# Optimization experiments

Measured on AMD Instinct MI355X. Metric: run time of the kernel, lower is better.

The kernel has to match this reference:

```python
import jax, jax.numpy as jnp
import numpy as np

N, G, E, H, M = 200000, 16, 400000, 400000, 800000
DN, DG, DE, DH, DM = 128, 32, 128, 64, 64
K_EDGE, K_HYP, AK = 32, 3, 8  # fixed incident edges per node, nodes per hyperedge, attention key size / heads
LN_EPS = 1e-3  # keras LayerNormalization default epsilon


def setup_inputs() -> dict:
    key = jax.random.key(0)
    ks = jax.random.split(key, 20)
    p = lambda k, shp: (0.02 * jax.random.normal(k, shp, dtype=jnp.float32))
    return {
        "nodes": jax.random.normal(ks[0], (N, DN), dtype=jnp.float32),
        "globals_": jax.random.normal(ks[1], (G, DG), dtype=jnp.float32),
        "n_node": jnp.full((G,), N // G, dtype=jnp.int32),
        "edges": jax.random.normal(ks[2], (E, DE), dtype=jnp.float32),
        "edge_ind": jax.random.randint(ks[3], (N, K_EDGE), 0, E, dtype=jnp.int32),
        "hfeat": jax.random.normal(ks[4], (H, DH), dtype=jnp.float32),
        "hind": jax.random.randint(ks[5], (H, K_HYP), 0, N, dtype=jnp.int32),
        "mfeat": jax.random.normal(ks[6], (M, DM), dtype=jnp.float32),
        "mind": jax.random.randint(ks[7], (M,), 0, N, dtype=jnp.int32),
        "Wq": p(ks[8], (DN, AK)), "bq": jnp.zeros((AK,), jnp.float32),
        "Wk": p(ks[9], (DE, AK)), "bk": jnp.zeros((AK,), jnp.float32),
        "Wc": p(ks[10], (4, AK, AK)), "bc": jnp.zeros((AK,), jnp.float32),
        "W1": p(ks[11], (DN + DG + AK + DH + DM, 256)), "b1": jnp.zeros((256,), jnp.float32),
        "W2": p(ks[12], (256, 128)), "b2": jnp.zeros((128,), jnp.float32),
        "ln_g": jnp.ones((128,), jnp.float32), "ln_b": jnp.zeros((128,), jnp.float32),
    }


def reference(nodes, globals_, n_node, edges, edge_ind, hfeat, hind, mfeat, mind,
              Wq, bq, Wk, bk, Wc, bc, W1, b1, W2, b2, ln_g, ln_b):
    n = nodes.shape[0]
    # _one_to_segments: repeat globals per node (graph id from n_node offsets)
    gid = jnp.searchsorted(jnp.cumsum(n_node), jnp.arange(n), side="right")
    g_per_node = globals_[gid]  # [N, DG]

    # EDGES branch: fixed-number multi-head attention over incident edges
    q = nodes @ Wq + bq   # [N, AK]
    k = edges @ Wk + bk   # [E, AK]
    # Conv1D(kernel=4, 'same') on a length-1 sequence: only kernel tap 1 touches data
    q_mh = q @ Wc[1] + bc  # [N, heads]
    k_mh = k @ Wc[1] + bc  # [E, heads]
    ek = k_mh[edge_ind]                         # [N, K, heads] gathered keys (= values)
    attn = jax.nn.softmax(q_mh[:, None, :] * ek, axis=1)
    edge_agg = jnp.sum(attn * ek, axis=1)       # [N, heads] (flatten of [N,1,heads])

    # _one_to_fixed_number: scatter hyperedge features to their K_HYP member nodes
    hh, kk, dh = hfeat.shape[0], hind.shape[1], hfeat.shape[1]
    h_agg = jax.ops.segment_sum(
        jnp.broadcast_to(hfeat[:, None, :], (hh, kk, dh)).reshape(hh * kk, dh),
        hind.reshape(-1), num_segments=n)       # [N, DH]

    # _one_to_unsorted_segments
    m_agg = jax.ops.segment_sum(mfeat, mind, num_segments=n)  # [N, DM]

    x = jnp.concatenate([nodes, g_per_node, edge_agg, h_agg, m_agg], axis=1)
    h1 = jax.nn.relu(x @ W1 + b1)
    h2 = jax.nn.relu(h1 @ W2 + b2)
    mu = jnp.mean(h2, axis=-1, keepdims=True)
    var = jnp.var(h2, axis=-1, keepdims=True)
    out = (h2 - mu) * jax.lax.rsqrt(var + LN_EPS) * ln_g + ln_b
    return out
```

## Files before the change

### kernel.cpp

```cpp
#include <hip/hip_runtime.h>
#include <hip/hip_bf16.h>
#include <math.h>

#define N_NODES 200000
#define N_E     400000
#define N_H     400000
#define N_M     800000
#define HK3     1200000
#define DIM_N   128
#define K_EDGE  32
#define D1      296
#define KX      320
#define LN_EPS  1e-3f
#define TILE    32
#define CHUNK   1024
#define NCH     196

typedef __attribute__((ext_vector_type(8))) short bf16x8;
typedef __attribute__((ext_vector_type(4))) float f32x4;
typedef unsigned short ushort_t;

#define SWZ(rr) (((rr) & 7) << 4)

__device__ __forceinline__ short f2bf(float f) {
    unsigned u = __float_as_uint(f);
    unsigned r = (u + 0x7fffu + ((u >> 16) & 1u)) >> 16;
    return (short)r;
}
__device__ __forceinline__ float bf2f(ushort_t u) {
    return __uint_as_float(((unsigned)u) << 16);
}
__device__ __forceinline__ void split2(float v, short& hi, short& lo) {
    hi = f2bf(v);
    float r = v - __uint_as_float(((unsigned)(ushort_t)hi) << 16);
    lo = f2bf(r);
}

__global__ void prep_weights(const float* __restrict__ Wq, const float* __restrict__ bq,
                             const float* __restrict__ Wk, const float* __restrict__ bk,
                             const float* __restrict__ Wc, const float* __restrict__ bc,
                             float* Wqc, float* bqc, float* Wkc, float* bkc) {
    int t = blockIdx.x * 256 + threadIdx.x;
    const float* Wc1 = Wc + 64;
    if (t < 128 * 8) {
        int i = t >> 3, o = t & 7;
        float s = 0.f, s2 = 0.f;
        for (int a = 0; a < 8; ++a) {
            float w = Wc1[a * 8 + o];
            s  += Wq[i * 8 + a] * w;
            s2 += Wk[i * 8 + a] * w;
        }
        Wqc[t] = s;
        Wkc[t] = s2;
    } else if (t < 128 * 8 + 8) {
        int o = t - 1024;
        float s = 0.f, s2 = 0.f;
        for (int a = 0; a < 8; ++a) {
            float w = Wc1[a * 8 + o];
            s  += bq[a] * w;
            s2 += bk[a] * w;
        }
        bqc[o] = s + bc[o];
        bkc[o] = s2 + bc[o];
    }
}

__global__ void prep_wF(const float* __restrict__ W1, const float* __restrict__ W2,
                        short* __restrict__ W1Fh, short* __restrict__ W1Fl,
                        short* __restrict__ W2Fh, short* __restrict__ W2Fl) {
    int g = blockIdx.x * 256 + threadIdx.x;
    if (g < 10240) {
        int l = g & 63, f = g >> 6;
        int s = f % 10, nt = (f / 10) & 3, wid = f / 40;
        int col = wid * 64 + nt * 16 + (l & 15);
        int k0 = s * 32 + (l >> 4) * 8;
        #pragma unroll
        for (int j = 0; j < 8; ++j) {
            int k = k0 + j;
            float w = (k < D1) ? W1[k * 256 + col] : 0.f;
            short hi, lo; split2(w, hi, lo);
            W1Fh[g * 8 + j] = hi; W1Fl[g * 8 + j] = lo;
        }
    } else if (g < 14336) {
        int u = g - 10240;
        int l = u & 63, f = u >> 6;
        int s = f & 7, nt = (f >> 3) & 1, wid = f >> 4;
        int col = wid * 32 + nt * 16 + (l & 15);
        int k0 = s * 32 + (l >> 4) * 8;
        #pragma unroll
        for (int j = 0; j < 8; ++j) {
            float w = W2[(k0 + j) * 128 + col];
            short hi, lo; split2(w, hi, lo);
            W2Fh[u * 8 + j] = hi; W2Fl[u * 8 + j] = lo;
        }
    }
}

__global__ __launch_bounds__(256) void mh_kernel(const float* __restrict__ feat,
                                                 const float* __restrict__ Wf,
                                                 const float* __restrict__ bf_,
                                                 ushort_t* __restrict__ out8) {
    __shared__ __align__(16) float el[32 * 132];
    __shared__ __align__(16) float wlT[8 * 132];
    __shared__ float bl[8];
    int tid = threadIdx.x;
    for (int i = tid; i < 1024; i += 256) {
        int h = i >> 7, k = i & 127;
        wlT[h * 132 + k] = Wf[k * 8 + h];
    }
    if (tid < 8) bl[tid] = bf_[tid];
    long e0 = (long)blockIdx.x * 32;
    const float4* ep = (const float4*)feat + e0 * 32;
    for (int it = 0; it < 4; ++it) {
        int idx = it * 256 + tid;
        int e = idx >> 5, f = idx & 31;
        float4 v = ep[e * 32 + f];
        float* d = &el[e * 132 + f * 4];
        d[0] = v.x; d[1] = v.y; d[2] = v.z; d[3] = v.w;
    }
    __syncthreads();
    int e = tid >> 3, h = tid & 7;
    float acc = bl[h];
    const float* er = &el[e * 132];
    const float* wr = &wlT[h * 132];
    #pragma unroll 8
    for (int i = 0; i < 128; i += 4) {
        float4 ev = *(const float4*)&er[i];
        float4 wv = *(const float4*)&wr[i];
        acc += ev.x * wv.x + ev.y * wv.y + ev.z * wv.z + ev.w * wv.w;
    }
    out8[(e0 + e) * 8 + h] = (ushort_t)f2bf(acc);
}

__global__ void zero_ints(int* __restrict__ p, int n) {
    int stride = gridDim.x * blockDim.x;
    for (int i = blockIdx.x * blockDim.x + threadIdx.x; i < n; i += stride) p[i] = 0;
}

__global__ void count_kernel(const int* __restrict__ hind, const int* __restrict__ mind,
                             int* __restrict__ cnth, int* __restrict__ cntm) {
    int t = blockIdx.x * 256 + threadIdx.x;
    if (t < HK3)              atomicAdd(&cnth[hind[t]], 1);
    else if (t < HK3 + N_M)   atomicAdd(&cntm[mind[t - HK3]], 1);
}

__global__ __launch_bounds__(256) void sum_chunks(const int* __restrict__ cnth,
                                                  const int* __restrict__ cntm,
                                                  int* __restrict__ bsum) {
    int b = blockIdx.x;
    const int* cnt = (b < NCH) ? cnth : cntm;
    int base = ((b < NCH) ? b : b - NCH) * CHUNK;
    int tid = threadIdx.x;
    int s = 0;
    #pragma unroll
    for (int i = 0; i < 4; ++i) {
        int idx = base + i * 256 + tid;
        if (idx < N_NODES) s += cnt[idx];
    }
    __shared__ int sb[4];
    for (int d = 1; d < 64; d <<= 1) s += __shfl_xor(s, d);
    if ((tid & 63) == 0) sb[tid >> 6] = s;
    __syncthreads();
    if (tid == 0) bsum[b] = sb[0] + sb[1] + sb[2] + sb[3];
}

__global__ __launch_bounds__(256) void scan_sums(int* __restrict__ bsum) {
    __shared__ int sh[2][256];
    int tid = threadIdx.x;
    sh[0][tid] = (tid < NCH) ? bsum[tid] : 0;
    sh[1][tid] = (tid < NCH) ? bsum[NCH + tid] : 0;
    __syncthreads();
    for (int d = 1; d < 256; d <<= 1) {
        int v0 = (tid >= d) ? sh[0][tid - d] : 0;
        int v1 = (tid >= d) ? sh[1][tid - d] : 0;
        __syncthreads();
        sh[0][tid] += v0; sh[1][tid] += v1;
        __syncthreads();
    }
    if (tid < NCH) {
        bsum[tid]       = tid ? sh[0][tid - 1] : 0;
        bsum[NCH + tid] = tid ? sh[1][tid - 1] : 0;
    }
}

__global__ __launch_bounds__(256) void scan_chunks(const int* __restrict__ cnth,
                                                   const int* __restrict__ cntm,
                                                   const int* __restrict__ bsum,
                                                   int* __restrict__ offh, int* __restrict__ woffh,
                                                   int* __restrict__ offm, int* __restrict__ woffm) {
    int b = blockIdx.x;
    bool ish = (b < NCH);
    const int* cnt = ish ? cnth : cntm;
    int c = ish ? b : b - NCH;
    int* off  = ish ? offh  : offm;
    int* woff = ish ? woffh : woffm;
    int base = c * CHUNK;
    int tid = threadIdx.x;
    __shared__ int lds[CHUNK];
    __shared__ int tsum[256];
    #pragma unroll
    for (int i = 0; i < 4; ++i) {
        int idx = base + i * 256 + tid;
        lds[i * 256 + tid] = (idx < N_NODES) ? cnt[idx] : 0;
    }
    __syncthreads();
    int v0 = lds[tid * 4], v1 = lds[tid * 4 + 1], v2 = lds[tid * 4 + 2], v3 = lds[tid * 4 + 3];
    int tot = v0 + v1 + v2 + v3;
    tsum[tid] = tot;
    __syncthreads();
    for (int d = 1; d < 256; d <<= 1) {
        int v = (tid >= d) ? tsum[tid - d] : 0;
        __syncthreads();
        tsum[tid] += v;
        __syncthreads();
    }
    int pre = tsum[tid] - tot + bsum[b];
    int4 o;
    o.x = pre; o.y = pre + v0; o.z = pre + v0 + v1; o.w = pre + v0 + v1 + v2;
    int idx = base + tid * 4;
    if (idx + 3 < N_NODES) {
        *(int4*)(off + idx)  = o;
        *(int4*)(woff + idx) = o;
    } else {
        if (idx     < N_NODES) { off[idx]     = o.x; woff[idx]     = o.x; }
        if (idx + 1 < N_NODES) { off[idx + 1] = o.y; woff[idx + 1] = o.y; }
        if (idx + 2 < N_NODES) { off[idx + 2] = o.z; woff[idx + 2] = o.z; }
        if (idx + 3 < N_NODES) { off[idx + 3] = o.w; woff[idx + 3] = o.w; }
    }
}

__global__ void fill_kernel(const int* __restrict__ hind, const int* __restrict__ mind,
                            int* __restrict__ woffh, int* __restrict__ woffm,
                            int* __restrict__ listh, int* __restrict__ listm) {
    int t = blockIdx.x * 256 + threadIdx.x;
    if (t < HK3) {
        int node = hind[t];
        int pos = atomicAdd(&woffh[node], 1);
        listh[pos] = t / 3;
    } else if (t < HK3 + N_M) {
        int m = t - HK3;
        int node = mind[m];
        int pos = atomicAdd(&woffm[node], 1);
        listm[pos] = m;
    }
}

__global__ __launch_bounds__(256) void main_kernel(
    const float* __restrict__ nodes, const float* __restrict__ globals_,
    const int* __restrict__ n_node, const int* __restrict__ edge_ind,
    const ushort_t* __restrict__ kmh, const ushort_t* __restrict__ qmh,
    const float* __restrict__ hfeat, const int* __restrict__ offh,
    const int* __restrict__ woffh, const int* __restrict__ listh,
    const float* __restrict__ mfeat, const int* __restrict__ offm,
    const int* __restrict__ woffm, const int* __restrict__ listm,
    const short* __restrict__ W1Fh, const short* __restrict__ W1Fl, const float* __restrict__ b1,
    const short* __restrict__ W2Fh, const short* __restrict__ W2Fl, const float* __restrict__ b2,
    const float* __restrict__ ln_g, const float* __restrict__ ln_b,
    float* __restrict__ out)
{
    __shared__ __align__(16) char buf[32768];
    __shared__ int eind[32 * 33];
    __shared__ float mrs[64];

    int tid = threadIdx.x;
    int n0 = blockIdx.x * TILE;
    char* xhi = buf;

    const float4* np4 = (const float4*)nodes;
    #pragma unroll
    for (int it = 0; it < 4; ++it) {
        int idx = it * 256 + tid;
        int r = idx >> 5, c4 = idx & 31;
        float4 v = np4[(size_t)(n0 + r) * 32 + c4];
        short4 hi;
        hi.x = f2bf(v.x); hi.y = f2bf(v.y); hi.z = f2bf(v.z); hi.w = f2bf(v.w);
        *(short4*)(xhi + r * 640 + ((c4 * 8) ^ SWZ(r))) = hi;
    }
    {
        int nn0 = n_node[0];
        int r = tid >> 3, c4 = tid & 7;
        int gid = (n0 + r) / nn0;
        float4 v = ((const float4*)globals_)[gid * 8 + c4];
        short4 hi;
        hi.x = f2bf(v.x); hi.y = f2bf(v.y); hi.z = f2bf(v.z); hi.w = f2bf(v.w);
        *(short4*)(xhi + r * 640 + ((256 + c4 * 8) ^ SWZ(r))) = hi;
    }
    {
        int r = tid >> 3, q = tid & 7;
        int n = n0 + r;
        float a[8];
        #pragma unroll
        for (int i = 0; i < 8; ++i) a[i] = 0.f;
        int e0 = offh[n], e1 = woffh[n];
        int e = e0;
        #define ACC8(U, V) do { \
            a[0] += (U).x; a[1] += (U).y; a[2] += (U).z; a[3] += (U).w; \
            a[4] += (V).x; a[5] += (V).y; a[6] += (V).z; a[7] += (V).w; } while (0)
        for (; e + 4 <= e1; e += 4) {
            int i0 = listh[e], i1 = listh[e + 1], i2 = listh[e + 2], i3 = listh[e + 3];
            const float4* p0 = (const float4*)(hfeat + (size_t)i0 * 64 + q * 8);
            const float4* p1 = (const float4*)(hfeat + (size_t)i1 * 64 + q * 8);
            const float4* p2 = (const float4*)(hfeat + (size_t)i2 * 64 + q * 8);
            const float4* p3 = (const float4*)(hfeat + (size_t)i3 * 64 + q * 8);
            float4 u0 = p0[0], v0 = p0[1];
            float4 u1 = p1[0], v1 = p1[1];
            float4 u2 = p2[0], v2 = p2[1];
            float4 u3 = p3[0], v3 = p3[1];
            ACC8(u0, v0); ACC8(u1, v1); ACC8(u2, v2); ACC8(u3, v3);
        }
        for (; e < e1; ++e) {
            const float4* p = (const float4*)(hfeat + (size_t)listh[e] * 64 + q * 8);
            float4 u = p[0], v = p[1];
            ACC8(u, v);
        }
        {
            bf16x8 hi;
            #pragma unroll
            for (int i = 0; i < 8; ++i) hi[i] = f2bf(a[i]);
            *(bf16x8*)(xhi + r * 640 + ((336 + q * 16) ^ SWZ(r))) = hi;
        }
        #pragma unroll
        for (int i = 0; i < 8; ++i) a[i] = 0.f;
        e0 = offm[n]; e1 = woffm[n];
        e = e0;
        for (; e + 4 <= e1; e += 4) {
            int i0 = listm[e], i1 = listm[e + 1], i2 = listm[e + 2], i3 = listm[e + 3];
            const float4* p0 = (const float4*)(mfeat + (size_t)i0 * 64 + q * 8);
            const float4* p1 = (const float4*)(mfeat + (size_t)i1 * 64 + q * 8);
            const float4* p2 = (const float4*)(mfeat + (size_t)i2 * 64 + q * 8);
            const float4* p3 = (const float4*)(mfeat + (size_t)i3 * 64 + q * 8);
            float4 u0 = p0[0], v0 = p0[1];
            float4 u1 = p1[0], v1 = p1[1];
            float4 u2 = p2[0], v2 = p2[1];
            float4 u3 = p3[0], v3 = p3[1];
            ACC8(u0, v0); ACC8(u1, v1); ACC8(u2, v2); ACC8(u3, v3);
        }
        for (; e < e1; ++e) {
            const float4* p = (const float4*)(mfeat + (size_t)listm[e] * 64 + q * 8);
            float4 u = p[0], v = p[1];
            ACC8(u, v);
        }
        #undef ACC8
        {
            bf16x8 hi;
            #pragma unroll
            for (int i = 0; i < 8; ++i) hi[i] = f2bf(a[i]);
            *(bf16x8*)(xhi + r * 640 + ((464 + q * 16) ^ SWZ(r))) = hi;
        }
    }
    if (tid < 192) {
        short4 z = { 0, 0, 0, 0 };
        int r = tid / 6, j = tid % 6;
        *(short4*)(xhi + r * 640 + ((592 + j * 8) ^ SWZ(r))) = z;
    }
    #pragma unroll
    for (int it = 0; it < 4; ++it) {
        int idx = it * 256 + tid;
        int r = idx >> 5, j = idx & 31;
        eind[r * 33 + j] = edge_ind[(size_t)(n0 + r) * 32 + j];
    }
    __syncthreads();

    {
        int r = tid & 31, h = tid >> 5;
        float qv = bf2f(qmh[(size_t)(n0 + r) * 8 + h]);
        float m = -INFINITY, s = 0.f, wv = 0.f;
        for (int j = 0; j < K_EDGE; ++j) {
            int e = eind[r * 33 + j];
            float v = bf2f(kmh[(size_t)e * 8 + h]);
            float l = qv * v;
            float mn = fmaxf(m, l);
            float fac = __expf(m - mn);
            float p = __expf(l - mn);
            s = s * fac + p;
            wv = wv * fac + p * v;
            m = mn;
        }
        *(short*)(xhi + r * 640 + ((320 + h * 2) ^ SWZ(r))) = f2bf(wv / s);
    }
    __syncthreads();

    int wid = tid >> 6, lane = tid & 63;
    int arow = lane & 15, kgrp = lane >> 4;
    f32x4 c1[2][4];
    #pragma unroll
    for (int mt = 0; mt < 2; ++mt)
        #pragma unroll
        for (int nt = 0; nt < 4; ++nt)
            c1[mt][nt] = (f32x4){0.f, 0.f, 0.f, 0.f};
    const bf16x8* w1h = (const bf16x8*)W1Fh;
    const bf16x8* w1l = (const bf16x8*)W1Fl;
    for (int s = 0; s < 10; ++s) {
        int kb = (s * 32 + kgrp * 8) * 2;
        bf16x8 ahv[2], bh[4], bl[4];
        #pragma unroll
        for (int mt = 0; mt < 2; ++mt) {
            int rr = mt * 16 + arow;
            ahv[mt] = *(const bf16x8*)(xhi + rr * 640 + (kb ^ SWZ(rr)));
        }
        #pragma unroll
        for (int nt = 0; nt < 4; ++nt) {
            size_t fi = ((size_t)(wid * 4 + nt) * 10 + s) * 64 + lane;
            bh[nt] = w1h[fi];
            bl[nt] = w1l[fi];
        }
        #pragma unroll
        for (int mt = 0; mt < 2; ++mt)
            #pragma unroll
            for (int nt = 0; nt < 4; ++nt) {
                c1[mt][nt] = __builtin_amdgcn_mfma_f32_16x16x32_bf16(ahv[mt], bh[nt], c1[mt][nt], 0, 0, 0);
                c1[mt][nt] = __builtin_amdgcn_mfma_f32_16x16x32_bf16(ahv[mt], bl[nt], c1[mt][nt], 0, 0, 0);
            }
    }
    __syncthreads();
    char* h1hi = buf;
    char* h1lo = buf + 16384;
    #pragma unroll
    for (int nt = 0; nt < 4; ++nt) {
        int col = wid * 64 + nt * 16 + arow;
        float bb = b1[col];
        #pragma unroll
        for (int mt = 0; mt < 2; ++mt)
            #pragma unroll
            for (int i = 0; i < 4; ++i) {
                int rr = mt * 16 + kgrp * 4 + i;
                float v = fmaxf(c1[mt][nt][i] + bb, 0.f);
                short hi, lo; split2(v, hi, lo);
                int off = rr * 512 + ((col * 2) ^ SWZ(rr));
                *(short*)(h1hi + off) = hi;
                *(short*)(h1lo + off) = lo;
            }
    }
    __syncthreads();

    f32x4 c2[2][2];
    #pragma unroll
    for (int mt = 0; mt < 2; ++mt)
        #pragma unroll
        for (int nt = 0; nt < 2; ++nt)
            c2[mt][nt] = (f32x4){0.f, 0.f, 0.f, 0.f};
    const bf16x8* w2h = (const bf16x8*)W2Fh;
    const bf16x8* w2l = (const bf16x8*)W2Fl;
    for (int s = 0; s < 8; ++s) {
        int kb = (s * 32 + kgrp * 8) * 2;
        bf16x8 ahv[2], alv[2], bh[2], bl[2];
        #pragma unroll
        for (int mt = 0; mt < 2; ++mt) {
            int rr = mt * 16 + arow;
            int off = rr * 512 + (kb ^ SWZ(rr));
            ahv[mt] = *(const bf16x8*)(h1hi + off);
            alv[mt] = *(const bf16x8*)(h1lo + off);
        }
        #pragma unroll
        for (int nt = 0; nt < 2; ++nt) {
            size_t fi = ((size_t)(wid * 2 + nt) * 8 + s) * 64 + lane;
            bh[nt] = w2h[fi];
            bl[nt] = w2l[fi];
        }
        #pragma unroll
        for (int mt = 0; mt < 2; ++mt)
            #pragma unroll
            for (int nt = 0; nt < 2; ++nt) {
                c2[mt][nt] = __builtin_amdgcn_mfma_f32_16x16x32_bf16(ahv[mt], bh[nt], c2[mt][nt], 0, 0, 0);
                c2[mt][nt] = __builtin_amdgcn_mfma_f32_16x16x32_bf16(ahv[mt], bl[nt], c2[mt][nt], 0, 0, 0);
                c2[mt][nt] = __builtin_amdgcn_mfma_f32_16x16x32_bf16(alv[mt], bh[nt], c2[mt][nt], 0, 0, 0);
            }
    }
    __syncthreads();
    #pragma unroll
    for (int nt = 0; nt < 2; ++nt) {
        int col = wid * 32 + nt * 16 + arow;
        float bb = b2[col];
        #pragma unroll
        for (int mt = 0; mt < 2; ++mt)
            #pragma unroll
            for (int i = 0; i < 4; ++i) {
                int rr = mt * 16 + kgrp * 4 + i;
                *(float*)(buf + rr * 528 + col * 4) = fmaxf(c2[mt][nt][i] + bb, 0.f);
            }
    }
    __syncthreads();

    {
        int r = tid >> 3, q = tid & 7;
        const float* row = (const float*)(buf + r * 528) + q * 16;
        float s = 0.f, sq = 0.f;
        #pragma unroll
        for (int j = 0; j < 4; ++j) {
            float4 v = *(const float4*)(row + j * 4);
            s  += v.x + v.y + v.z + v.w;
            sq += v.x * v.x + v.y * v.y + v.z * v.z + v.w * v.w;
        }
        s  += __shfl_xor(s, 1);  sq += __shfl_xor(sq, 1);
        s  += __shfl_xor(s, 2);  sq += __shfl_xor(sq, 2);
        s  += __shfl_xor(s, 4);  sq += __shfl_xor(sq, 4);
        if (q == 0) {
            float mean = s * (1.f / 128.f);
            float var = sq * (1.f / 128.f) - mean * mean;
            mrs[r] = mean;
            mrs[32 + r] = rsqrtf(var + LN_EPS);
        }
    }
    __syncthreads();
    #pragma unroll
    for (int it = 0; it < 4; ++it) {
        int idx = it * 256 + tid;
        int r = idx >> 5, c4 = idx & 31;
        float4 v = *(const float4*)(buf + r * 528 + c4 * 16);
        float mu = mrs[r], rs = mrs[32 + r];
        float4 g = ((const float4*)ln_g)[c4];
        float4 bb = ((const float4*)ln_b)[c4];
        float4 o;
        o.x = (v.x - mu) * rs * g.x + bb.x;
        o.y = (v.y - mu) * rs * g.y + bb.y;
        o.z = (v.z - mu) * rs * g.z + bb.z;
        o.w = (v.w - mu) * rs * g.w + bb.w;
        ((float4*)out)[(size_t)(n0 + r) * 32 + c4] = o;
    }
}

extern "C" void kernel_launch(void* const* d_in, const int* in_sizes, int n_in,
                              void* d_out, int out_size, void* d_ws, size_t ws_size,
                              hipStream_t stream) {
    const float* nodes    = (const float*)d_in[0];
    const float* globals_ = (const float*)d_in[1];
    const int*   n_node   = (const int*)  d_in[2];
    const float* edges    = (const float*)d_in[3];
    const int*   edge_ind = (const int*)  d_in[4];
    const float* hfeat    = (const float*)d_in[5];
    const int*   hind     = (const int*)  d_in[6];
    const float* mfeat    = (const float*)d_in[7];
    const int*   mind     = (const int*)  d_in[8];
    const float* Wq       = (const float*)d_in[9];
    const float* bq       = (const float*)d_in[10];
    const float* Wk       = (const float*)d_in[11];
    const float* bk       = (const float*)d_in[12];
    const float* Wc       = (const float*)d_in[13];
    const float* bc       = (const float*)d_in[14];
    const float* W1       = (const float*)d_in[15];
    const float* b1       = (const float*)d_in[16];
    const float* W2       = (const float*)d_in[17];
    const float* b2       = (const float*)d_in[18];
    const float* ln_g     = (const float*)d_in[19];
    const float* ln_b     = (const float*)d_in[20];
    float* out = (float*)d_out;

    char* w = (char*)d_ws;
    size_t off = 0;
    auto take = [&](size_t bytes) -> char* {
        char* p = w + off;
        off = (off + bytes + 255) & ~(size_t)255;
        return p;
    };
    float*    Wqc  = (float*)take(1024 * 4);
    float*    bqc  = (float*)take(8 * 4);
    float*    Wkc  = (float*)take(1024 * 4);
    float*    bkc  = (float*)take(8 * 4);
    short*    W1Fh = (short*)take(256 * KX * 2);
    short*    W1Fl = (short*)take(256 * KX * 2);
    short*    W2Fh = (short*)take(128 * 256 * 2);
    short*    W2Fl = (short*)take(128 * 256 * 2);
    ushort_t* kmh  = (ushort_t*)take((size_t)N_E * 8 * 2);
    ushort_t* qmh  = (ushort_t*)take((size_t)N_NODES * 8 * 2);
    int*      cnth = (int*)take((size_t)N_NODES * 4);
    int*      cntm = (int*)take((size_t)N_NODES * 4);
    int*      offh = (int*)take((size_t)N_NODES * 4);
    int*      woffh= (int*)take((size_t)N_NODES * 4);
    int*      offm = (int*)take((size_t)N_NODES * 4);
    int*      woffm= (int*)take((size_t)N_NODES * 4);
    int*      listh= (int*)take((size_t)HK3 * 4);
    int*      listm= (int*)take((size_t)N_M * 4);
    int*      bsum = (int*)take(2 * NCH * 4);
    (void)ws_size;

    prep_weights<<<5, 256, 0, stream>>>(Wq, bq, Wk, bk, Wc, bc, Wqc, bqc, Wkc, bkc);
    prep_wF<<<56, 256, 0, stream>>>(W1, W2, W1Fh, W1Fl, W2Fh, W2Fl);
    mh_kernel<<<N_E / 32, 256, 0, stream>>>(edges, Wkc, bkc, kmh);
    mh_kernel<<<N_NODES / 32, 256, 0, stream>>>(nodes, Wqc, bqc, qmh);
    zero_ints<<<512, 256, 0, stream>>>(cnth, 2 * N_NODES);
    count_kernel<<<(HK3 + N_M + 255) / 256, 256, 0, stream>>>(hind, mind, cnth, cntm);
    sum_chunks<<<2 * NCH, 256, 0, stream>>>(cnth, cntm, bsum);
    scan_sums<<<1, 256, 0, stream>>>(bsum);
    scan_chunks<<<2 * NCH, 256, 0, stream>>>(cnth, cntm, bsum, offh, woffh, offm, woffm);
    fill_kernel<<<(HK3 + N_M + 255) / 256, 256, 0, stream>>>(hind, mind, woffh, woffm, listh, listm);
    main_kernel<<<N_NODES / TILE, 256, 0, stream>>>(
        nodes, globals_, n_node, edge_ind, kmh, qmh,
        hfeat, offh, woffh, listh, mfeat, offm, woffm, listm,
        W1Fh, W1Fl, b1, W2Fh, W2Fl, b2, ln_g, ln_b, out);
}
```

Baseline: 713.4 us.

## Fuse projection and count kernels into one launch; drop h1 low-part split

The two per-row head-projection launches and the atomic count launch are merged into one kernel whose blocks are partitioned by index range, so independent work can overlap and launch gaps disappear. Separately, the second MLP layer no longer splits h1 into hi/lo bf16 parts: h1 is stored once as bf16, and one of the three MFMA passes is removed, along with 12KB of shared memory. This cuts LDS traffic, MFMA count and LDS footprint, which may raise occupancy, at the cost of lower precision in the h1 activations.

```diff
diff --git a/kernel.cpp b/kernel.cpp
--- a/kernel.cpp
+++ b/kernel.cpp
@@ -15,6 +15,9 @@
 #define TILE    32
 #define CHUNK   1024
 #define NCH     196
+#define NB_E    12500
+#define NB_N    6250
+#define NB_C    7813
 
 typedef __attribute__((ext_vector_type(8))) short bf16x8;
 typedef __attribute__((ext_vector_type(4))) float f32x4;
@@ -96,20 +99,18 @@
     }
 }
 
-__global__ __launch_bounds__(256) void mh_kernel(const float* __restrict__ feat,
-                                                 const float* __restrict__ Wf,
-                                                 const float* __restrict__ bf_,
-                                                 ushort_t* __restrict__ out8) {
-    __shared__ __align__(16) float el[32 * 132];
-    __shared__ __align__(16) float wlT[8 * 132];
-    __shared__ float bl[8];
-    int tid = threadIdx.x;
+__device__ __forceinline__ void mh_body(const float* __restrict__ feat,
+                                        const float* __restrict__ Wf,
+                                        const float* __restrict__ bf_,
+                                        ushort_t* __restrict__ out8,
+                                        int blk, int tid,
+                                        float* el, float* wlT, float* bl) {
     for (int i = tid; i < 1024; i += 256) {
         int h = i >> 7, k = i & 127;
         wlT[h * 132 + k] = Wf[k * 8 + h];
     }
     if (tid < 8) bl[tid] = bf_[tid];
-    long e0 = (long)blockIdx.x * 32;
+    long e0 = (long)blk * 32;
     const float4* ep = (const float4*)feat + e0 * 32;
     for (int it = 0; it < 4; ++it) {
         int idx = it * 256 + tid;
@@ -132,16 +133,32 @@
     out8[(e0 + e) * 8 + h] = (ushort_t)f2bf(acc);
 }
 
+__global__ __launch_bounds__(256) void aux1_kernel(
+    const float* __restrict__ edges, const float* __restrict__ Wkc,
+    const float* __restrict__ bkc, ushort_t* __restrict__ kmh,
+    const float* __restrict__ nodes, const float* __restrict__ Wqc,
+    const float* __restrict__ bqc, ushort_t* __restrict__ qmh,
+    const int* __restrict__ hind, const int* __restrict__ mind,
+    int* __restrict__ cnth, int* __restrict__ cntm)
+{
+    __shared__ __align__(16) float el[32 * 132];
+    __shared__ __align__(16) float wlT[8 * 132];
+    __shared__ float bl[8];
+    int b = blockIdx.x, tid = threadIdx.x;
+    if (b < NB_E) {
+        mh_body(edges, Wkc, bkc, kmh, b, tid, el, wlT, bl);
+    } else if (b < NB_E + NB_N) {
+        mh_body(nodes, Wqc, bqc, qmh, b - NB_E, tid, el, wlT, bl);
+    } else {
+        int t = (b - NB_E - NB_N) * 256 + tid;
+        if (t < HK3)              atomicAdd(&cnth[hind[t]], 1);
+        else if (t < HK3 + N_M)   atomicAdd(&cntm[mind[t - HK3]], 1);
+    }
+}
+
 __global__ void zero_ints(int* __restrict__ p, int n) {
     int stride = gridDim.x * blockDim.x;
     for (int i = blockIdx.x * blockDim.x + threadIdx.x; i < n; i += stride) p[i] = 0;
-}
-
-__global__ void count_kernel(const int* __restrict__ hind, const int* __restrict__ mind,
-                             int* __restrict__ cnth, int* __restrict__ cntm) {
-    int t = blockIdx.x * 256 + threadIdx.x;
-    if (t < HK3)              atomicAdd(&cnth[hind[t]], 1);
-    else if (t < HK3 + N_M)   atomicAdd(&cntm[mind[t - HK3]], 1);
 }
 
 __global__ __launch_bounds__(256) void sum_chunks(const int* __restrict__ cnth,
@@ -258,7 +275,7 @@
     const float* __restrict__ ln_g, const float* __restrict__ ln_b,
     float* __restrict__ out)
 {
-    __shared__ __align__(16) char buf[32768];
+    __shared__ __align__(16) char buf[20480];
     __shared__ int eind[32 * 33];
     __shared__ float mrs[64];
 
@@ -413,8 +430,7 @@
             }
     }
     __syncthreads();
-    char* h1hi = buf;
-    char* h1lo = buf + 16384;
+    char* h1p = buf;
     #pragma unroll
     for (int nt = 0; nt < 4; ++nt) {
         int col = wid * 64 + nt * 16 + arow;
@@ -425,10 +441,7 @@
             for (int i = 0; i < 4; ++i) {
                 int rr = mt * 16 + kgrp * 4 + i;
                 float v = fmaxf(c1[mt][nt][i] + bb, 0.f);
-                short hi, lo; split2(v, hi, lo);
-                int off = rr * 512 + ((col * 2) ^ SWZ(rr));
-                *(short*)(h1hi + off) = hi;
-                *(short*)(h1lo + off) = lo;
+                *(short*)(h1p + rr * 512 + ((col * 2) ^ SWZ(rr))) = f2bf(v);
             }
     }
     __syncthreads();
@@ -443,13 +456,11 @@
     const bf16x8* w2l = (const bf16x8*)W2Fl;
     for (int s = 0; s < 8; ++s) {
         int kb = (s * 32 + kgrp * 8) * 2;
-        bf16x8 ahv[2], alv[2], bh[2], bl[2];
+        bf16x8 ahv[2], bh[2], bl[2];
         #pragma unroll
         for (int mt = 0; mt < 2; ++mt) {
             int rr = mt * 16 + arow;
-            int off = rr * 512 + (kb ^ SWZ(rr));
-            ahv[mt] = *(const bf16x8*)(h1hi + off);
-            alv[mt] = *(const bf16x8*)(h1lo + off);
+            ahv[mt] = *(const bf16x8*)(h1p + rr * 512 + (kb ^ SWZ(rr)));
         }
         #pragma unroll
         for (int nt = 0; nt < 2; ++nt) {
@@ -463,7 +474,6 @@
             for (int nt = 0; nt < 2; ++nt) {
                 c2[mt][nt] = __builtin_amdgcn_mfma_f32_16x16x32_bf16(ahv[mt], bh[nt], c2[mt][nt], 0, 0, 0);
                 c2[mt][nt] = __builtin_amdgcn_mfma_f32_16x16x32_bf16(ahv[mt], bl[nt], c2[mt][nt], 0, 0, 0);
-                c2[mt][nt] = __builtin_amdgcn_mfma_f32_16x16x32_bf16(alv[mt], bh[nt], c2[mt][nt], 0, 0, 0);
             }
     }
     __syncthreads();
@@ -575,10 +585,9 @@
 
     prep_weights<<<5, 256, 0, stream>>>(Wq, bq, Wk, bk, Wc, bc, Wqc, bqc, Wkc, bkc);
     prep_wF<<<56, 256, 0, stream>>>(W1, W2, W1Fh, W1Fl, W2Fh, W2Fl);
-    mh_kernel<<<N_E / 32, 256, 0, stream>>>(edges, Wkc, bkc, kmh);
-    mh_kernel<<<N_NODES / 32, 256, 0, stream>>>(nodes, Wqc, bqc, qmh);
     zero_ints<<<512, 256, 0, stream>>>(cnth, 2 * N_NODES);
-    count_kernel<<<(HK3 + N_M + 255) / 256, 256, 0, stream>>>(hind, mind, cnth, cntm);
+    aux1_kernel<<<NB_E + NB_N + NB_C, 256, 0, stream>>>(
+        edges, Wkc, bkc, kmh, nodes, Wqc, bqc, qmh, hind, mind, cnth, cntm);
     sum_chunks<<<2 * NCH, 256, 0, stream>>>(cnth, cntm, bsum);
     scan_sums<<<1, 256, 0, stream>>>(bsum);
     scan_chunks<<<2 * NCH, 256, 0, stream>>>(cnth, cntm, bsum, offh, woffh, offm, woffm);
```

Measured after the change: 691.1 us. -3.1%, faster.
